# Optimization experiments

Measured on AMD Instinct MI355X. Metric: run time of the kernel, lower is better.

## Reference

```python
import jax, jax.numpy as jnp
import numpy as np

N = 50000
E = 400000
IN_DIM = 384
HID = 256
Q_DIM = 384
HEAD_HID = 128


def _glorot(key, shape):
    fan_in, fan_out = shape[0], shape[1]
    lim = float(np.sqrt(6.0 / (fan_in + fan_out)))
    return jax.random.uniform(key, shape, jnp.float32, -lim, lim)


def setup_inputs() -> dict:
    key = jax.random.key(0)
    ks = jax.random.split(key, 10)
    x = jax.random.normal(ks[0], (N, IN_DIM), jnp.float32)
    edge_index = jax.random.randint(ks[1], (2, E), 0, N, dtype=jnp.int64)
    q = jax.random.normal(ks[2], (Q_DIM,), jnp.float32)
    # layer 1: Linear(in_dim*2 + query_dim -> hidden)
    W1 = _glorot(ks[3], (IN_DIM * 2 + Q_DIM, HID))
    b1 = jnp.zeros((HID,), jnp.float32)
    # layer 2: Linear(hidden*2 + query_dim -> hidden)
    W2 = _glorot(ks[4], (HID * 2 + Q_DIM, HID))
    b2 = jnp.zeros((HID,), jnp.float32)
    # score head: Linear(hidden + query_dim -> 128) -> ReLU -> Linear(128 -> 1)
    Wh1 = _glorot(ks[5], (HID + Q_DIM, HEAD_HID))
    bh1 = jnp.zeros((HEAD_HID,), jnp.float32)
    Wh2 = _glorot(ks[6], (HEAD_HID, 1))
    bh2 = jnp.zeros((1,), jnp.float32)
    return {"x": x, "edge_index": edge_index, "q": q,
            "W1": W1, "b1": b1, "W2": W2, "b2": b2,
            "Wh1": Wh1, "bh1": bh1, "Wh2": Wh2, "bh2": bh2}


def _sage_layer(h, src, dst, q, W, b, n_nodes):
    # mean aggregation with self-loops: (sum_{j in N(i)} h_j + h_i) / (deg_i + 1)
    deg = jnp.zeros((n_nodes,), h.dtype).at[dst].add(1.0) + 1.0  # [N]
    agg = (jax.ops.segment_sum(h[src], dst, num_segments=n_nodes) + h) / deg[:, None]
    q_exp = jnp.broadcast_to(q, (n_nodes, q.shape[0]))
    cat = jnp.concatenate([h, agg, q_exp], axis=-1)  # [N, 2*d + q_dim]
    return jax.nn.relu(cat @ W + b)  # dropout is identity in eval mode


def reference(x, edge_index, q, W1, b1, W2, b2, Wh1, bh1, Wh2, bh2):
    src, dst = edge_index[0], edge_index[1]
    n = x.shape[0]
    h = _sage_layer(x, src, dst, q, W1, b1, n)
    h = _sage_layer(h, src, dst, q, W2, b2, n)
    q_exp = jnp.broadcast_to(q, (n, q.shape[0]))
    s = jax.nn.relu(jnp.concatenate([h, q_exp], axis=-1) @ Wh1 + bh1)
    logits = (s @ Wh2 + bh2).squeeze(-1)  # [N]
    return logits
```

## Files before the change

kernel.cpp:

```cpp
#include <hip/hip_runtime.h>
#include <cstdint>
#include <cstddef>

typedef unsigned short u16;
typedef short short8 __attribute__((ext_vector_type(8)));
typedef unsigned short u16x8 __attribute__((ext_vector_type(8)));
typedef unsigned short u16x4 __attribute__((ext_vector_type(4)));
typedef float f32x4 __attribute__((ext_vector_type(4)));

#define DEVI __device__ __forceinline__

#if defined(__has_builtin)
#if __has_builtin(__builtin_amdgcn_global_load_lds)
#define USE_GLD 1
#endif
#endif

DEVI float bf2f(u16 u) { return __uint_as_float(((unsigned)u) << 16); }
DEVI u16 f2bf(float f) {
  unsigned u = __float_as_uint(f);
  u += 0x7FFFu + ((u >> 16) & 1u);
  return (u16)(u >> 16);
}

DEVI void stage16(const u16* __restrict__ g, u16* lds_base, int lane) {
#ifdef USE_GLD
  __builtin_amdgcn_global_load_lds(
      (const __attribute__((address_space(1))) unsigned int*)g,
      (__attribute__((address_space(3))) unsigned int*)lds_base, 16, 0, 0);
#else
  *(u16x8*)(lds_base + lane * 8) = *(const u16x8*)g;
#endif
}

__global__ void build_deg(const int* __restrict__ dst, int* __restrict__ deg, int E) {
  int e = blockIdx.x * 256 + threadIdx.x;
  if (e < E) atomicAdd(&deg[dst[e]], 1);
}

__global__ __launch_bounds__(256) void scan1(const int* __restrict__ deg,
                                             int* __restrict__ pref,
                                             int* __restrict__ bsum, int Nn) {
  __shared__ int wsum[4];
  int i = blockIdx.x * 256 + threadIdx.x;
  int lane = threadIdx.x & 63, w = threadIdx.x >> 6;
  int v = (i < Nn) ? deg[i] : 0;
  int s = v;
  for (int off = 1; off < 64; off <<= 1) {
    int t = __shfl_up(s, off, 64);
    if (lane >= off) s += t;
  }
  if (lane == 63) wsum[w] = s;
  __syncthreads();
  int add = 0;
  for (int k = 0; k < w; ++k) add += wsum[k];
  int incl = s + add;
  if (i < Nn) pref[i] = incl - v;
  if (threadIdx.x == 255) bsum[blockIdx.x] = incl;
}

__global__ __launch_bounds__(256) void scan2(int* __restrict__ bsum,
                                             int* __restrict__ row_ofs,
                                             int nb, int Nn) {
  __shared__ int wsum[4];
  int t = threadIdx.x;
  int lane = t & 63, w = t >> 6;
  int v = (t < nb) ? bsum[t] : 0;
  int s = v;
  for (int off = 1; off < 64; off <<= 1) {
    int u = __shfl_up(s, off, 64);
    if (lane >= off) s += u;
  }
  if (lane == 63) wsum[w] = s;
  __syncthreads();
  int add = 0;
  for (int k = 0; k < w; ++k) add += wsum[k];
  int incl = s + add;
  if (t < nb) bsum[t] = incl - v;
  if (t == 255) row_ofs[Nn] = incl;
}

__global__ __launch_bounds__(256) void scan3(const int* __restrict__ pref,
                                             const int* __restrict__ bsum,
                                             int* __restrict__ row_ofs,
                                             int* __restrict__ cursor, int Nn) {
  int i = blockIdx.x * 256 + threadIdx.x;
  if (i < Nn) {
    int r = pref[i] + bsum[blockIdx.x];
    row_ofs[i] = r;
    cursor[i] = r;
  }
}

__global__ void csr_fill(const int* __restrict__ src, const int* __restrict__ dst,
                         int* __restrict__ cursor, int* __restrict__ col, int E) {
  int e = blockIdx.x * 256 + threadIdx.x;
  if (e < E) {
    int p = atomicAdd(&cursor[dst[e]], 1);
    col[p] = src[e];
  }
}

__global__ void pack_bt(const float* __restrict__ W, u16* __restrict__ Bt,
                        int K, int ldW, int r1) {
  int c = blockIdx.y;
  int k = blockIdx.x * 256 + threadIdx.x;
  if (k >= K) return;
  float v = (c < ldW) ? W[(size_t)k * ldW + c]
                      : W[(size_t)(r1 + k) * ldW + (c - ldW)];
  Bt[(size_t)c * K + k] = f2bf(v);
}

__global__ __launch_bounds__(384) void bias_q(
    const float* __restrict__ W, const float* __restrict__ b,
    const float* __restrict__ q, float* __restrict__ outb,
    int ld, int roff, int Kq) {
  __shared__ float part[6];
  int c = blockIdx.x;
  int t = threadIdx.x;
  float p = (t < Kq) ? q[t] * W[(size_t)(roff + t) * ld + c] : 0.0f;
  for (int off = 32; off > 0; off >>= 1) p += __shfl_down(p, off, 64);
  if ((t & 63) == 0) part[t >> 6] = p;
  __syncthreads();
  if (t == 0) {
    float acc = b[c];
    int nw = (blockDim.x + 63) >> 6;
    for (int w = 0; w < nw; ++w) acc += part[w];
    outb[c] = acc;
  }
}

#define W_NC 512
#define ES 520

#define GEMM512_COMPUTE()                                                      \
  {                                                                            \
    short8 bfr[8];                                                             \
    _Pragma("unroll") for (int nt = 0; nt < 8; ++nt) bfr[nt] =                 \
        *(const short8*)&lds_b[((wave * 128 + nt * 16 + m) * 4 + csel) * 8];   \
    _Pragma("unroll") for (int mt = 0; mt < 4; ++mt) {                         \
      short8 af = *(const short8*)&lds_a[((mt * 16 + m) * 4 + csel) * 8];      \
      _Pragma("unroll") for (int nt = 0; nt < 8; ++nt)                         \
          acc[mt][nt] = __builtin_amdgcn_mfma_f32_16x16x32_bf16(               \
              af, bfr[nt], acc[mt][nt], 0, 0, 0);                              \
    }                                                                          \
  }

#define GEMM512_EPILOGUE()                                                     \
  {                                                                            \
    u16* et = lds_b;                                                           \
    _Pragma("unroll") for (int mt = 0; mt < 4; ++mt) {                         \
      __syncthreads();                                                         \
      _Pragma("unroll") for (int nt = 0; nt < 8; ++nt) {                       \
        int col = wave * 128 + nt * 16 + m;                                    \
        float bb = (col < bias_len) ? bias[col] : 0.0f;                        \
        _Pragma("unroll") for (int r = 0; r < 4; ++r) {                        \
          float v = acc[mt][nt][r] + bb;                                       \
          if (relu) v = fmaxf(v, 0.0f);                                        \
          et[(quad * 4 + r) * ES + col] = f2bf(v);                             \
        }                                                                      \
      }                                                                        \
      __syncthreads();                                                         \
      _Pragma("unroll") for (int p = 0; p < 4; ++p) {                          \
        int row_loc = p * 4 + wave;                                            \
        int grow = row0 + mt * 16 + row_loc;                                   \
        if (grow < M)                                                          \
          *(u16x8*)&C[(size_t)grow * W_NC + lane * 8] =                        \
              *(const u16x8*)&et[row_loc * ES + lane * 8];                     \
      }                                                                        \
    }                                                                          \
  }

#define GEMM512_B_SETUP()                                                      \
  const u16* pbB[8];                                                           \
  _Pragma("unroll") for (int p = 0; p < 8; ++p) {                              \
    int L = p * 256 + tid;                                                     \
    int c = L >> 2, qs = L & 3;                                                \
    int g = qs ^ ((c >> 1) & 3);                                               \
    pbB[p] = Bt + (size_t)c * K + g * 8;                                       \
  }

#define GEMM512_B_STAGE()                                                      \
  _Pragma("unroll") for (int p = 0; p < 8; ++p) {                              \
    stage16(pbB[p], lds_b + (size_t)(p * 256 + wave * 64) * 8, lane);          \
    pbB[p] += 32;                                                              \
  }

__global__ __launch_bounds__(256, 2) void gemm512_f32a(
    const float* __restrict__ A, const u16* __restrict__ Bt,
    u16* __restrict__ C, const float* __restrict__ bias,
    int M, int K, int bias_len, int relu) {
  __shared__ __align__(16) u16 lds_a[64 * 32];
  __shared__ __align__(16) u16 lds_b[512 * 32];

  const int tid = threadIdx.x;
  const int lane = tid & 63;
  const int wave = tid >> 6;
  const int row0 = blockIdx.x * 64;
  const int m = lane & 15;
  const int quad = lane >> 4;
  const int csel = quad ^ ((m >> 1) & 3);

  const int rA = tid >> 2;
  const int qA = tid & 3;
  const int sA = rA * 4 + (qA ^ ((rA >> 1) & 3));
  int ga = row0 + rA; if (ga >= M) ga = M - 1;
  const float* pa = A + (size_t)ga * K + qA * 8;

  GEMM512_B_SETUP()

  f32x4 acc[4][8] = {};

  f32x4 va0 = *(const f32x4*)pa, va1 = *(const f32x4*)(pa + 4);
  pa += 32;

  for (int k0 = 0; k0 < K; k0 += 32) {
    __syncthreads();
    GEMM512_B_STAGE()
    u16x8 h;
#pragma unroll
    for (int j = 0; j < 4; ++j) { h[j] = f2bf(va0[j]); h[j + 4] = f2bf(va1[j]); }
    *(u16x8*)&lds_a[sA * 8] = h;
    const float* pn = (k0 + 32 < K) ? pa : A;
    f32x4 na0 = *(const f32x4*)pn, na1 = *(const f32x4*)(pn + 4);
    pa += 32;
    __syncthreads();
    GEMM512_COMPUTE()
    va0 = na0; va1 = na1;
  }

  GEMM512_EPILOGUE()
}

__global__ __launch_bounds__(256, 2) void gemm512_bf16a(
    const u16* __restrict__ A, const u16* __restrict__ Bt,
    u16* __restrict__ C, const float* __restrict__ bias,
    int M, int K, int bias_len, int relu) {
  __shared__ __align__(16) u16 lds_a[64 * 32];
  __shared__ __align__(16) u16 lds_b[512 * 32];

  const int tid = threadIdx.x;
  const int lane = tid & 63;
  const int wave = tid >> 6;
  const int row0 = blockIdx.x * 64;
  const int m = lane & 15;
  const int quad = lane >> 4;
  const int csel = quad ^ ((m >> 1) & 3);

  const int rA = tid >> 2;
  const int qA = tid & 3;
  const int sA = rA * 4 + (qA ^ ((rA >> 1) & 3));
  int ga = row0 + rA; if (ga >= M) ga = M - 1;
  const u16* pa = A + (size_t)ga * K + qA * 8;

  GEMM512_B_SETUP()

  f32x4 acc[4][8] = {};

  u16x8 va = *(const u16x8*)pa;
  pa += 32;

  for (int k0 = 0; k0 < K; k0 += 32) {
    __syncthreads();
    GEMM512_B_STAGE()
    *(u16x8*)&lds_a[sA * 8] = va;
    const u16* pn = (k0 + 32 < K) ? pa : A;
    u16x8 na = *(const u16x8*)pn;
    pa += 32;
    __syncthreads();
    GEMM512_COMPUTE()
    va = na;
  }

  GEMM512_EPILOGUE()
}

#define BM 128
#define BN 128
#define BK 32
#define ELD_STRIDE 136

__global__ __launch_bounds__(256) void gemm_bf16a(
    const u16* __restrict__ A, const u16* __restrict__ Bt,
    u16* __restrict__ C, const float* __restrict__ bias,
    int M, int K, int Nc, int bias_len, int relu) {
  __shared__ __align__(16) u16 lds[64 * ELD_STRIDE];
  u16* lds_a = lds;
  u16* lds_b = lds + BM * BK;

  const int tid = threadIdx.x;
  const int lane = tid & 63;
  const int wave = tid >> 6;
  const int wm = wave & 1, wn = wave >> 1;
  const int row0 = blockIdx.y * BM;
  const int col0 = blockIdx.x * BN;
  const int m = lane & 15;
  const int quad = lane >> 4;
  const int csel = quad ^ ((m >> 1) & 3);

  const int r0 = tid >> 2, r1 = 64 + r0;
  const int cs = tid & 3;
  const int s0 = r0 * 4 + (cs ^ ((r0 >> 1) & 3));
  const int s1 = r1 * 4 + (cs ^ ((r1 >> 1) & 3));
  const int cb0 = cs ^ ((r0 >> 1) & 3);
  const int cb1 = cs ^ ((r1 >> 1) & 3);
  int ga0 = row0 + r0; if (ga0 >= M) ga0 = M - 1;
  int ga1 = row0 + r1; if (ga1 >= M) ga1 = M - 1;
  const u16* pa0 = A + (size_t)ga0 * K + cs * 8;
  const u16* pa1 = A + (size_t)ga1 * K + cs * 8;
  const u16* pb0 = Bt + (size_t)(col0 + r0) * K + cb0 * 8;
  const u16* pb1 = Bt + (size_t)(col0 + r1) * K + cb1 * 8;
  u16* lb0 = lds_b + (size_t)(wave * 64) * 8;
  u16* lb1 = lds_b + (size_t)(256 + wave * 64) * 8;

  f32x4 acc[4][4] = {};

  u16x8 va0 = *(const u16x8*)pa0; pa0 += BK;
  u16x8 va1 = *(const u16x8*)pa1; pa1 += BK;

  for (int k0 = 0; k0 < K; k0 += BK) {
    __syncthreads();
    stage16(pb0, lb0, lane); pb0 += BK;
    stage16(pb1, lb1, lane); pb1 += BK;
    *(u16x8*)&lds_a[s0 * 8] = va0;
    *(u16x8*)&lds_a[s1 * 8] = va1;
    const u16* n0 = (k0 + BK < K) ? pa0 : A;
    const u16* n1 = (k0 + BK < K) ? pa1 : A;
    u16x8 w0 = *(const u16x8*)n0;
    u16x8 w1 = *(const u16x8*)n1;
    pa0 += BK; pa1 += BK;
    __syncthreads();

    short8 af[4], bfv[4];
#pragma unroll
    for (int mt = 0; mt < 4; ++mt)
      af[mt] = *(const short8*)&lds_a[((wm * 64 + mt * 16 + m) * 4 + csel) * 8];
#pragma unroll
    for (int nt = 0; nt < 4; ++nt)
      bfv[nt] = *(const short8*)&lds_b[((wn * 64 + nt * 16 + m) * 4 + csel) * 8];
#pragma unroll
    for (int mt = 0; mt < 4; ++mt)
#pragma unroll
      for (int nt = 0; nt < 4; ++nt)
        acc[mt][nt] = __builtin_amdgcn_mfma_f32_16x16x32_bf16(
            af[mt], bfv[nt], acc[mt][nt], 0, 0, 0);
    va0 = w0; va1 = w1;
  }

  {
    const int rr = tid >> 4;
    const int cseg = tid & 15;
#pragma unroll
    for (int h = 0; h < 2; ++h) {
      __syncthreads();
      if (wm == h) {
#pragma unroll
        for (int nt = 0; nt < 4; ++nt) {
          int col_loc = wn * 64 + nt * 16 + m;
          float bb = (col0 + col_loc < bias_len) ? bias[col0 + col_loc] : 0.0f;
#pragma unroll
          for (int mt = 0; mt < 4; ++mt)
#pragma unroll
            for (int r = 0; r < 4; ++r) {
              float v = acc[mt][nt][r] + bb;
              if (relu) v = fmaxf(v, 0.0f);
              lds[(mt * 16 + quad * 4 + r) * ELD_STRIDE + col_loc] = f2bf(v);
            }
        }
      }
      __syncthreads();
#pragma unroll
      for (int p = 0; p < 4; ++p) {
        int row_loc = p * 16 + rr;
        int grow = row0 + h * 64 + row_loc;
        if (grow < M)
          *(u16x8*)&C[(size_t)grow * Nc + col0 + cseg * 8] =
              *(const u16x8*)&lds[row_loc * ELD_STRIDE + cseg * 8];
      }
    }
  }
}

__global__ __launch_bounds__(256) void aggregate(
    const u16* __restrict__ C, const int* __restrict__ row_ofs,
    const int* __restrict__ col_idx, u16* __restrict__ H, int Nn) {
  int node = blockIdx.x * 4 + (threadIdx.x >> 6);
  if (node >= Nn) return;
  int lane = threadIdx.x & 63;
  int s = row_ofs[node], e = row_ofs[node + 1];
  float inv = 1.0f / (float)(e - s + 1);
  const u16* crow = C + (size_t)node * 512;
  u16x4 y0 = *(const u16x4*)(crow + 256 + lane * 4);
  float a0 = bf2f(y0[0]), a1 = bf2f(y0[1]), a2 = bf2f(y0[2]), a3 = bf2f(y0[3]);
  int t = s;
  for (; t + 4 <= e; t += 4) {
    int j0 = col_idx[t], j1 = col_idx[t + 1], j2 = col_idx[t + 2], j3 = col_idx[t + 3];
    u16x4 v0 = *(const u16x4*)(C + (size_t)j0 * 512 + 256 + lane * 4);
    u16x4 v1 = *(const u16x4*)(C + (size_t)j1 * 512 + 256 + lane * 4);
    u16x4 v2 = *(const u16x4*)(C + (size_t)j2 * 512 + 256 + lane * 4);
    u16x4 v3 = *(const u16x4*)(C + (size_t)j3 * 512 + 256 + lane * 4);
    a0 += bf2f(v0[0]) + bf2f(v1[0]) + bf2f(v2[0]) + bf2f(v3[0]);
    a1 += bf2f(v0[1]) + bf2f(v1[1]) + bf2f(v2[1]) + bf2f(v3[1]);
    a2 += bf2f(v0[2]) + bf2f(v1[2]) + bf2f(v2[2]) + bf2f(v3[2]);
    a3 += bf2f(v0[3]) + bf2f(v1[3]) + bf2f(v2[3]) + bf2f(v3[3]);
  }
  for (; t < e; ++t) {
    int j = col_idx[t];
    u16x4 yj = *(const u16x4*)(C + (size_t)j * 512 + 256 + lane * 4);
    a0 += bf2f(yj[0]); a1 += bf2f(yj[1]); a2 += bf2f(yj[2]); a3 += bf2f(yj[3]);
  }
  u16x4 u = *(const u16x4*)(crow + lane * 4);
  u16x4 o;
  o[0] = f2bf(fmaxf(bf2f(u[0]) + a0 * inv, 0.0f));
  o[1] = f2bf(fmaxf(bf2f(u[1]) + a1 * inv, 0.0f));
  o[2] = f2bf(fmaxf(bf2f(u[2]) + a2 * inv, 0.0f));
  o[3] = f2bf(fmaxf(bf2f(u[3]) + a3 * inv, 0.0f));
  *(u16x4*)(H + (size_t)node * 256 + lane * 4) = o;
}

__global__ __launch_bounds__(256) void head_final(
    const u16* __restrict__ S, const float* __restrict__ Wh2,
    const float* __restrict__ bh2, float* __restrict__ out, int Nn) {
  int node = blockIdx.x * 4 + (threadIdx.x >> 6);
  if (node >= Nn) return;
  int lane = threadIdx.x & 63;
  const u16* srow = S + (size_t)node * 128 + lane * 2;
  float v = bf2f(srow[0]) * Wh2[lane * 2] + bf2f(srow[1]) * Wh2[lane * 2 + 1];
  for (int off = 32; off > 0; off >>= 1) v += __shfl_down(v, off, 64);
  if (lane == 0) out[node] = v + bh2[0];
}

extern "C" void kernel_launch(void* const* d_in, const int* in_sizes, int n_in,
                              void* d_out, int out_size, void* d_ws, size_t ws_size,
                              hipStream_t stream) {
  const float* x   = (const float*)d_in[0];
  const int*   ei  = (const int*)d_in[1];
  const float* q   = (const float*)d_in[2];
  const float* W1  = (const float*)d_in[3];
  const float* b1  = (const float*)d_in[4];
  const float* W2  = (const float*)d_in[5];
  const float* b2  = (const float*)d_in[6];
  const float* Wh1 = (const float*)d_in[7];
  const float* bh1 = (const float*)d_in[8];
  const float* Wh2 = (const float*)d_in[9];
  const float* bh2 = (const float*)d_in[10];

  const int N = in_sizes[0] / 384;
  const int E = in_sizes[1] / 2;
  const int Npad = ((N + 127) / 128) * 128;
  const int* esrc = ei;
  const int* edst = ei + E;

  size_t off = 0;
  auto alloc = [&](size_t bytes) -> void* {
    void* p = (char*)d_ws + off;
    off += (bytes + 255) & ~(size_t)255;
    return p;
  };
  int* deg     = (int*)alloc((size_t)N * 4);
  int* row_ofs = (int*)alloc((size_t)(N + 1) * 4);
  int* cursor  = (int*)alloc((size_t)N * 4);
  int* colidx  = (int*)alloc((size_t)E * 4);
  int* pref    = (int*)alloc((size_t)N * 4);
  int* bsum    = (int*)alloc(256 * 4);
  u16* B1t = (u16*)alloc((size_t)512 * 384 * 2);
  u16* B2t = (u16*)alloc((size_t)512 * 256 * 2);
  u16* Bht = (u16*)alloc((size_t)128 * 256 * 2);
  float* cq1 = (float*)alloc(256 * 4);
  float* cq2 = (float*)alloc(256 * 4);
  float* cqh = (float*)alloc(128 * 4);
  u16* Cbuf = (u16*)alloc((size_t)Npad * 512 * 2);
  u16* Hbuf = (u16*)alloc((size_t)Npad * 256 * 2);

  (void)hipMemsetAsync(deg, 0, (size_t)N * 4, stream);
  int eb = (E + 255) / 256;
  int nb = (N + 255) / 256;
  build_deg<<<eb, 256, 0, stream>>>(edst, deg, E);
  scan1<<<nb, 256, 0, stream>>>(deg, pref, bsum, N);
  scan2<<<1, 256, 0, stream>>>(bsum, row_ofs, nb, N);
  scan3<<<nb, 256, 0, stream>>>(pref, bsum, row_ofs, cursor, N);
  csr_fill<<<eb, 256, 0, stream>>>(esrc, edst, cursor, colidx, E);

  pack_bt<<<dim3(2, 512), 256, 0, stream>>>(W1, B1t, 384, 256, 384);
  pack_bt<<<dim3(1, 512), 256, 0, stream>>>(W2, B2t, 256, 256, 256);
  pack_bt<<<dim3(1, 128), 256, 0, stream>>>(Wh1, Bht, 256, 128, 0);
  bias_q<<<256, 384, 0, stream>>>(W1, b1, q, cq1, 256, 768, 384);
  bias_q<<<256, 384, 0, stream>>>(W2, b2, q, cq2, 256, 512, 384);
  bias_q<<<128, 384, 0, stream>>>(Wh1, bh1, q, cqh, 128, 256, 384);

  int gb64 = (N + 63) / 64;
  int mb = Npad / 128;
  int nb4 = (N + 3) / 4;
  gemm512_f32a<<<gb64, 256, 0, stream>>>(x, B1t, Cbuf, cq1, N, 384, 256, 0);
  aggregate<<<nb4, 256, 0, stream>>>(Cbuf, row_ofs, colidx, Hbuf, N);
  gemm512_bf16a<<<gb64, 256, 0, stream>>>(Hbuf, B2t, Cbuf, cq2, N, 256, 256, 0);
  aggregate<<<nb4, 256, 0, stream>>>(Cbuf, row_ofs, colidx, Hbuf, N);
  gemm_bf16a<<<dim3(1, mb), 256, 0, stream>>>(Hbuf, Bht, Cbuf, cqh, N, 256, 128, 128, 1);
  head_final<<<nb4, 256, 0, stream>>>(Cbuf, Wh2, bh2, (float*)d_out, N);
}
```

Before: 368.9 us.

## Fuse head GEMM with final dot, merge setup kernels, double K-step in GEMMs

The head GEMM epilogue now applies bias, ReLU and the Wh2 dot product in registers, reduces across lanes and waves, and writes logits directly. This removes the intermediate S buffer and the separate head_final kernel. The three pack kernels and the three bias kernels are each merged into one launch to cut launch overhead. The two 512-wide GEMMs now stage two 32-wide K slices per barrier pair using doubled LDS. That halves the syncs but raises LDS use, which may reduce occupancy.

```diff
diff --git a/kernel.cpp b/kernel.cpp
--- a/kernel.cpp
+++ b/kernel.cpp
@@ -101,45 +101,71 @@
   }
 }
 
-__global__ void pack_bt(const float* __restrict__ W, u16* __restrict__ Bt,
-                        int K, int ldW, int r1) {
-  int c = blockIdx.y;
-  int k = blockIdx.x * 256 + threadIdx.x;
-  if (k >= K) return;
-  float v = (c < ldW) ? W[(size_t)k * ldW + c]
-                      : W[(size_t)(r1 + k) * ldW + (c - ldW)];
-  Bt[(size_t)c * K + k] = f2bf(v);
-}
-
-__global__ __launch_bounds__(384) void bias_q(
-    const float* __restrict__ W, const float* __restrict__ b,
-    const float* __restrict__ q, float* __restrict__ outb,
-    int ld, int roff, int Kq) {
+__global__ __launch_bounds__(256) void pack_all(
+    const float* __restrict__ W1, const float* __restrict__ W2,
+    const float* __restrict__ Wh1, u16* __restrict__ B1t,
+    u16* __restrict__ B2t, u16* __restrict__ Bht) {
+  int b = blockIdx.x;
+  if (b < 1024) {
+    int c = b >> 1;
+    int k = (b & 1) * 256 + threadIdx.x;
+    if (k < 384) {
+      float v = (c < 256) ? W1[(size_t)k * 256 + c]
+                          : W1[(size_t)(384 + k) * 256 + (c - 256)];
+      B1t[(size_t)c * 384 + k] = f2bf(v);
+    }
+  } else if (b < 1536) {
+    int c = b - 1024;
+    int k = threadIdx.x;
+    float v = (c < 256) ? W2[(size_t)k * 256 + c]
+                        : W2[(size_t)(256 + k) * 256 + (c - 256)];
+    B2t[(size_t)c * 256 + k] = f2bf(v);
+  } else {
+    int c = b - 1536;
+    int k = threadIdx.x;
+    Bht[(size_t)c * 256 + k] = f2bf(Wh1[(size_t)k * 128 + c]);
+  }
+}
+
+__global__ __launch_bounds__(384) void bias_all(
+    const float* __restrict__ W1, const float* __restrict__ b1,
+    const float* __restrict__ W2, const float* __restrict__ b2,
+    const float* __restrict__ Wh1, const float* __restrict__ bh1,
+    const float* __restrict__ q, float* __restrict__ cq1,
+    float* __restrict__ cq2, float* __restrict__ cqh) {
   __shared__ float part[6];
-  int c = blockIdx.x;
+  int b = blockIdx.x;
+  const float* W; const float* bb; float* o; int ld, roff, c;
+  if (b < 256)      { W = W1;  bb = b1;  o = cq1; ld = 256; roff = 768; c = b; }
+  else if (b < 512) { W = W2;  bb = b2;  o = cq2; ld = 256; roff = 512; c = b - 256; }
+  else              { W = Wh1; bb = bh1; o = cqh; ld = 128; roff = 256; c = b - 512; }
   int t = threadIdx.x;
-  float p = (t < Kq) ? q[t] * W[(size_t)(roff + t) * ld + c] : 0.0f;
+  float p = q[t] * W[(size_t)(roff + t) * ld + c];
   for (int off = 32; off > 0; off >>= 1) p += __shfl_down(p, off, 64);
   if ((t & 63) == 0) part[t >> 6] = p;
   __syncthreads();
   if (t == 0) {
-    float acc = b[c];
-    int nw = (blockDim.x + 63) >> 6;
-    for (int w = 0; w < nw; ++w) acc += part[w];
-    outb[c] = acc;
+    float acc = bb[c];
+    for (int w = 0; w < 6; ++w) acc += part[w];
+    o[c] = acc;
   }
 }
 
 #define W_NC 512
 #define ES 520
-
-#define GEMM512_COMPUTE()                                                      \
+#define OFF_A0 0
+#define OFF_A1 (64 * 32)
+#define OFF_B0 (2 * 64 * 32)
+#define OFF_B1 (2 * 64 * 32 + 512 * 32)
+#define SMEM_TOT (2 * 64 * 32 + 2 * 512 * 32)
+
+#define GEMM512_COMPUTE(LA, LB)                                                \
   {                                                                            \
     short8 bfr[8];                                                             \
     _Pragma("unroll") for (int nt = 0; nt < 8; ++nt) bfr[nt] =                 \
-        *(const short8*)&lds_b[((wave * 128 + nt * 16 + m) * 4 + csel) * 8];   \
+        *(const short8*)&(LB)[((wave * 128 + nt * 16 + m) * 4 + csel) * 8];    \
     _Pragma("unroll") for (int mt = 0; mt < 4; ++mt) {                         \
-      short8 af = *(const short8*)&lds_a[((mt * 16 + m) * 4 + csel) * 8];      \
+      short8 af = *(const short8*)&(LA)[((mt * 16 + m) * 4 + csel) * 8];       \
       _Pragma("unroll") for (int nt = 0; nt < 8; ++nt)                         \
           acc[mt][nt] = __builtin_amdgcn_mfma_f32_16x16x32_bf16(               \
               af, bfr[nt], acc[mt][nt], 0, 0, 0);                              \
@@ -148,7 +174,7 @@
 
 #define GEMM512_EPILOGUE()                                                     \
   {                                                                            \
-    u16* et = lds_b;                                                           \
+    u16* et = lds_b0;                                                          \
     _Pragma("unroll") for (int mt = 0; mt < 4; ++mt) {                         \
       __syncthreads();                                                         \
       _Pragma("unroll") for (int nt = 0; nt < 8; ++nt) {                       \
@@ -180,18 +206,23 @@
     pbB[p] = Bt + (size_t)c * K + g * 8;                                       \
   }
 
-#define GEMM512_B_STAGE()                                                      \
+#define GEMM512_B_STAGE2()                                                     \
   _Pragma("unroll") for (int p = 0; p < 8; ++p) {                              \
-    stage16(pbB[p], lds_b + (size_t)(p * 256 + wave * 64) * 8, lane);          \
-    pbB[p] += 32;                                                              \
+    u16* d = lds_b0 + (size_t)(p * 256 + wave * 64) * 8;                       \
+    stage16(pbB[p], d, lane);                                                  \
+    stage16(pbB[p] + 32, d + (512 * 32), lane);         \
+    pbB[p] += 64;                                                              \
   }
 
 __global__ __launch_bounds__(256, 2) void gemm512_f32a(
     const float* __restrict__ A, const u16* __restrict__ Bt,
     u16* __restrict__ C, const float* __restrict__ bias,
     int M, int K, int bias_len, int relu) {
-  __shared__ __align__(16) u16 lds_a[64 * 32];
-  __shared__ __align__(16) u16 lds_b[512 * 32];
+  __shared__ __align__(16) u16 smem[SMEM_TOT];
+  u16* lds_a0 = smem + OFF_A0;
+  u16* lds_a1 = smem + OFF_A1;
+  u16* lds_b0 = smem + OFF_B0;
+  u16* lds_b1 = smem + OFF_B1;
 
   const int tid = threadIdx.x;
   const int lane = tid & 63;
@@ -211,22 +242,29 @@
 
   f32x4 acc[4][8] = {};
 
-  f32x4 va0 = *(const f32x4*)pa, va1 = *(const f32x4*)(pa + 4);
-  pa += 32;
-
-  for (int k0 = 0; k0 < K; k0 += 32) {
+  f32x4 v0a = *(const f32x4*)pa, v0b = *(const f32x4*)(pa + 4);
+  f32x4 v1a = *(const f32x4*)(pa + 32), v1b = *(const f32x4*)(pa + 36);
+  pa += 64;
+
+  for (int k0 = 0; k0 < K; k0 += 64) {
     __syncthreads();
-    GEMM512_B_STAGE()
-    u16x8 h;
-#pragma unroll
-    for (int j = 0; j < 4; ++j) { h[j] = f2bf(va0[j]); h[j + 4] = f2bf(va1[j]); }
-    *(u16x8*)&lds_a[sA * 8] = h;
-    const float* pn = (k0 + 32 < K) ? pa : A;
-    f32x4 na0 = *(const f32x4*)pn, na1 = *(const f32x4*)(pn + 4);
-    pa += 32;
+    GEMM512_B_STAGE2()
+    u16x8 h0, h1;
+#pragma unroll
+    for (int j = 0; j < 4; ++j) {
+      h0[j] = f2bf(v0a[j]); h0[j + 4] = f2bf(v0b[j]);
+      h1[j] = f2bf(v1a[j]); h1[j + 4] = f2bf(v1b[j]);
+    }
+    *(u16x8*)&lds_a0[sA * 8] = h0;
+    *(u16x8*)&lds_a1[sA * 8] = h1;
+    const float* pn = (k0 + 64 < K) ? pa : A;
+    f32x4 n0a = *(const f32x4*)pn, n0b = *(const f32x4*)(pn + 4);
+    f32x4 n1a = *(const f32x4*)(pn + 32), n1b = *(const f32x4*)(pn + 36);
+    pa += 64;
     __syncthreads();
-    GEMM512_COMPUTE()
-    va0 = na0; va1 = na1;
+    GEMM512_COMPUTE(lds_a0, lds_b0)
+    GEMM512_COMPUTE(lds_a1, lds_b1)
+    v0a = n0a; v0b = n0b; v1a = n1a; v1b = n1b;
   }
 
   GEMM512_EPILOGUE()
@@ -236,8 +274,11 @@
     const u16* __restrict__ A, const u16* __restrict__ Bt,
     u16* __restrict__ C, const float* __restrict__ bias,
     int M, int K, int bias_len, int relu) {
-  __shared__ __align__(16) u16 lds_a[64 * 32];
-  __shared__ __align__(16) u16 lds_b[512 * 32];
+  __shared__ __align__(16) u16 smem[SMEM_TOT];
+  u16* lds_a0 = smem + OFF_A0;
+  u16* lds_a1 = smem + OFF_A1;
+  u16* lds_b0 = smem + OFF_B0;
+  u16* lds_b1 = smem + OFF_B1;
 
   const int tid = threadIdx.x;
   const int lane = tid & 63;
@@ -257,43 +298,44 @@
 
   f32x4 acc[4][8] = {};
 
-  u16x8 va = *(const u16x8*)pa;
-  pa += 32;
-
-  for (int k0 = 0; k0 < K; k0 += 32) {
+  u16x8 va0 = *(const u16x8*)pa;
+  u16x8 va1 = *(const u16x8*)(pa + 32);
+  pa += 64;
+
+  for (int k0 = 0; k0 < K; k0 += 64) {
     __syncthreads();
-    GEMM512_B_STAGE()
-    *(u16x8*)&lds_a[sA * 8] = va;
-    const u16* pn = (k0 + 32 < K) ? pa : A;
-    u16x8 na = *(const u16x8*)pn;
-    pa += 32;
+    GEMM512_B_STAGE2()
+    *(u16x8*)&lds_a0[sA * 8] = va0;
+    *(u16x8*)&lds_a1[sA * 8] = va1;
+    const u16* pn = (k0 + 64 < K) ? pa : A;
+    u16x8 na0 = *(const u16x8*)pn;
+    u16x8 na1 = *(const u16x8*)(pn + 32);
+    pa += 64;
     __syncthreads();
-    GEMM512_COMPUTE()
-    va = na;
+    GEMM512_COMPUTE(lds_a0, lds_b0)
+    GEMM512_COMPUTE(lds_a1, lds_b1)
+    va0 = na0; va1 = na1;
   }
 
   GEMM512_EPILOGUE()
 }
 
 #define BM 128
-#define BN 128
 #define BK 32
-#define ELD_STRIDE 136
-
-__global__ __launch_bounds__(256) void gemm_bf16a(
+
+__global__ __launch_bounds__(256) void gemm_head(
     const u16* __restrict__ A, const u16* __restrict__ Bt,
-    u16* __restrict__ C, const float* __restrict__ bias,
-    int M, int K, int Nc, int bias_len, int relu) {
-  __shared__ __align__(16) u16 lds[64 * ELD_STRIDE];
-  u16* lds_a = lds;
-  u16* lds_b = lds + BM * BK;
+    const float* __restrict__ cqh, const float* __restrict__ Wh2,
+    const float* __restrict__ bh2, float* __restrict__ out, int M, int K) {
+  __shared__ __align__(16) u16 lds_a[BM * BK];
+  __shared__ __align__(16) u16 lds_b[BM * BK];
+  __shared__ float red[128][2];
 
   const int tid = threadIdx.x;
   const int lane = tid & 63;
   const int wave = tid >> 6;
   const int wm = wave & 1, wn = wave >> 1;
-  const int row0 = blockIdx.y * BM;
-  const int col0 = blockIdx.x * BN;
+  const int row0 = blockIdx.x * BM;
   const int m = lane & 15;
   const int quad = lane >> 4;
   const int csel = quad ^ ((m >> 1) & 3);
@@ -308,8 +350,8 @@
   int ga1 = row0 + r1; if (ga1 >= M) ga1 = M - 1;
   const u16* pa0 = A + (size_t)ga0 * K + cs * 8;
   const u16* pa1 = A + (size_t)ga1 * K + cs * 8;
-  const u16* pb0 = Bt + (size_t)(col0 + r0) * K + cb0 * 8;
-  const u16* pb1 = Bt + (size_t)(col0 + r1) * K + cb1 * 8;
+  const u16* pb0 = Bt + (size_t)r0 * K + cb0 * 8;
+  const u16* pb1 = Bt + (size_t)r1 * K + cb1 * 8;
   u16* lb0 = lds_b + (size_t)(wave * 64) * 8;
   u16* lb1 = lds_b + (size_t)(256 + wave * 64) * 8;
 
@@ -347,37 +389,40 @@
     va0 = w0; va1 = w1;
   }
 
-  {
-    const int rr = tid >> 4;
-    const int cseg = tid & 15;
-#pragma unroll
-    for (int h = 0; h < 2; ++h) {
-      __syncthreads();
-      if (wm == h) {
-#pragma unroll
-        for (int nt = 0; nt < 4; ++nt) {
-          int col_loc = wn * 64 + nt * 16 + m;
-          float bb = (col0 + col_loc < bias_len) ? bias[col0 + col_loc] : 0.0f;
-#pragma unroll
-          for (int mt = 0; mt < 4; ++mt)
-#pragma unroll
-            for (int r = 0; r < 4; ++r) {
-              float v = acc[mt][nt][r] + bb;
-              if (relu) v = fmaxf(v, 0.0f);
-              lds[(mt * 16 + quad * 4 + r) * ELD_STRIDE + col_loc] = f2bf(v);
-            }
-        }
-      }
-      __syncthreads();
-#pragma unroll
-      for (int p = 0; p < 4; ++p) {
-        int row_loc = p * 16 + rr;
-        int grow = row0 + h * 64 + row_loc;
-        if (grow < M)
-          *(u16x8*)&C[(size_t)grow * Nc + col0 + cseg * 8] =
-              *(const u16x8*)&lds[row_loc * ELD_STRIDE + cseg * 8];
-      }
-    }
+  float part[4][4];
+#pragma unroll
+  for (int mt = 0; mt < 4; ++mt)
+#pragma unroll
+    for (int r = 0; r < 4; ++r) part[mt][r] = 0.0f;
+#pragma unroll
+  for (int nt = 0; nt < 4; ++nt) {
+    int col = wn * 64 + nt * 16 + m;
+    float bb = cqh[col];
+    float w2 = Wh2[col];
+#pragma unroll
+    for (int mt = 0; mt < 4; ++mt)
+#pragma unroll
+      for (int r = 0; r < 4; ++r)
+        part[mt][r] += fmaxf(acc[mt][nt][r] + bb, 0.0f) * w2;
+  }
+#pragma unroll
+  for (int off = 8; off > 0; off >>= 1)
+#pragma unroll
+    for (int mt = 0; mt < 4; ++mt)
+#pragma unroll
+      for (int r = 0; r < 4; ++r)
+        part[mt][r] += __shfl_xor(part[mt][r], off, 64);
+  if (m == 0) {
+#pragma unroll
+    for (int mt = 0; mt < 4; ++mt)
+#pragma unroll
+      for (int r = 0; r < 4; ++r)
+        red[wm * 64 + mt * 16 + quad * 4 + r][wn] = part[mt][r];
+  }
+  __syncthreads();
+  if (tid < 128) {
+    int grow = row0 + tid;
+    if (grow < M) out[grow] = red[tid][0] + red[tid][1] + bh2[0];
   }
 }
 
@@ -418,18 +463,6 @@
   *(u16x4*)(H + (size_t)node * 256 + lane * 4) = o;
 }
 
-__global__ __launch_bounds__(256) void head_final(
-    const u16* __restrict__ S, const float* __restrict__ Wh2,
-    const float* __restrict__ bh2, float* __restrict__ out, int Nn) {
-  int node = blockIdx.x * 4 + (threadIdx.x >> 6);
-  if (node >= Nn) return;
-  int lane = threadIdx.x & 63;
-  const u16* srow = S + (size_t)node * 128 + lane * 2;
-  float v = bf2f(srow[0]) * Wh2[lane * 2] + bf2f(srow[1]) * Wh2[lane * 2 + 1];
-  for (int off = 32; off > 0; off >>= 1) v += __shfl_down(v, off, 64);
-  if (lane == 0) out[node] = v + bh2[0];
-}
-
 extern "C" void kernel_launch(void* const* d_in, const int* in_sizes, int n_in,
                               void* d_out, int out_size, void* d_ws, size_t ws_size,
                               hipStream_t stream) {
@@ -481,12 +514,8 @@
   scan3<<<nb, 256, 0, stream>>>(pref, bsum, row_ofs, cursor, N);
   csr_fill<<<eb, 256, 0, stream>>>(esrc, edst, cursor, colidx, E);
 
-  pack_bt<<<dim3(2, 512), 256, 0, stream>>>(W1, B1t, 384, 256, 384);
-  pack_bt<<<dim3(1, 512), 256, 0, stream>>>(W2, B2t, 256, 256, 256);
-  pack_bt<<<dim3(1, 128), 256, 0, stream>>>(Wh1, Bht, 256, 128, 0);
-  bias_q<<<256, 384, 0, stream>>>(W1, b1, q, cq1, 256, 768, 384);
-  bias_q<<<256, 384, 0, stream>>>(W2, b2, q, cq2, 256, 512, 384);
-  bias_q<<<128, 384, 0, stream>>>(Wh1, bh1, q, cqh, 128, 256, 384);
+  pack_all<<<1664, 256, 0, stream>>>(W1, W2, Wh1, B1t, B2t, Bht);
+  bias_all<<<640, 384, 0, stream>>>(W1, b1, W2, b2, Wh1, bh1, q, cq1, cq2, cqh);
 
   int gb64 = (N + 63) / 64;
   int mb = Npad / 128;
@@ -495,6 +524,5 @@
   aggregate<<<nb4, 256, 0, stream>>>(Cbuf, row_ofs, colidx, Hbuf, N);
   gemm512_bf16a<<<gb64, 256, 0, stream>>>(Hbuf, B2t, Cbuf, cq2, N, 256, 256, 0);
   aggregate<<<nb4, 256, 0, stream>>>(Cbuf, row_ofs, colidx, Hbuf, N);
-  gemm_bf16a<<<dim3(1, mb), 256, 0, stream>>>(Hbuf, Bht, Cbuf, cqh, N, 256, 128, 128, 1);
-  head_final<<<nb4, 256, 0, stream>>>(Cbuf, Wh2, bh2, (float*)d_out, N);
-}
+  gemm_head<<<mb, 256, 0, stream>>>(Hbuf, Bht, cqh, Wh2, bh2, (float*)d_out, N, 256);
+}
```

After: 345.9 us. -6.2%, faster.
